# Performance work log

Measured on AMD Instinct MI355X. Metric: run time of the kernel, lower is better.

## Reference

```python
import jax, jax.numpy as jnp
import numpy as np

B, C_IN, C_OUT, H, W = 4, 128, 64, 64, 64


def setup_inputs() -> dict:
    key = jax.random.key(0)
    ks = jax.random.split(key, 10)
    s = 0.05
    return {
        "x": jax.random.normal(ks[0], (B, C_IN, H, W), dtype=jnp.float32),
        "Wf": jax.random.normal(ks[1], (C_OUT, C_IN), dtype=jnp.float32) * s,
        "bf": jax.random.normal(ks[2], (C_OUT,), dtype=jnp.float32) * s,
        "Wg": jax.random.normal(ks[3], (C_OUT, C_IN), dtype=jnp.float32) * s,
        "bg": jax.random.normal(ks[4], (C_OUT,), dtype=jnp.float32) * s,
        "Wh": jax.random.normal(ks[5], (C_OUT, C_IN), dtype=jnp.float32) * s,
        "bh": jax.random.normal(ks[6], (C_OUT,), dtype=jnp.float32) * s,
        "Wa": jax.random.normal(ks[7], (C_OUT, C_OUT), dtype=jnp.float32) * s,
        "ba": jax.random.normal(ks[8], (C_OUT,), dtype=jnp.float32) * s,
        "gamma": jnp.ones((1,), dtype=jnp.float32),
    }


def _conv1x1(W, b, xf):
    # xf: [B, Cin, N] -> [B, Cout, N]
    return jnp.einsum('oc,bcn->bon', W, xf) + b[None, :, None]


def reference(x, Wf, bf, Wg, bg, Wh, bh, Wa, ba, gamma):
    nb, nc, imgh, imgw = x.shape
    xf = x.reshape(nb, nc, imgh * imgw)            # [B, Cin, N]
    f = _conv1x1(Wf, bf, xf)                       # [B, Co, N]
    g = _conv1x1(Wg, bg, xf)
    h = _conv1x1(Wh, bh, xf)
    # s = f^T @ g : [B, N, N]
    s = jnp.einsum('bon,bom->bnm', f, g)
    beta = jax.nn.softmax(s, axis=-1)              # softmax over keys (last dim)
    # o = beta @ h^T : [B, N, Co]
    o = jnp.einsum('bnm,bom->bno', beta, h)
    o = jnp.swapaxes(o, 1, 2)                      # [B, Co, N]
    o = _conv1x1(Wa, ba, o)                        # attn_conv 1x1
    out = gamma * o.reshape(nb, -1, imgh, imgw)    # [B, Co, H, W]
    return out
```

## Files before the change

kernel.cpp:

```cpp
#include <hip/hip_runtime.h>
#include <math.h>

#define BATCH 4
#define CIN   128
#define CO    64
#define NPIX  4096
#define LOG2E 1.4426950408889634f

typedef unsigned int   uint_t;
typedef unsigned short ushort_t;
typedef __bf16 bfx8 __attribute__((ext_vector_type(8)));
typedef float  f32x4  __attribute__((ext_vector_type(4)));
typedef float  f32x16 __attribute__((ext_vector_type(16)));

#define MFMA(a,b,c)   __builtin_amdgcn_mfma_f32_16x16x32_bf16((a),(b),(c),0,0,0)
#define MFMA32(a,b,c) __builtin_amdgcn_mfma_f32_32x32x16_bf16((a),(b),(c),0,0,0)
#define BC8(x) __builtin_bit_cast(bfx8,(x))

#if __has_builtin(__builtin_amdgcn_exp2f)
#define EXP2(x) __builtin_amdgcn_exp2f(x)
#else
#define EXP2(x) exp2f(x)
#endif

static __device__ __forceinline__ ushort_t f2bf(float f) {
    uint_t u = __builtin_bit_cast(uint_t, f);
    u = (u + 0x7fffu + ((u >> 16) & 1u)) >> 16;
    return (ushort_t)u;
}
static __device__ __forceinline__ float bf2f(ushort_t h) {
    return __builtin_bit_cast(float, (uint_t)h << 16);
}
static __device__ __forceinline__ uint_t pk2(float a, float b) {
    return (uint_t)f2bf(a) | ((uint_t)f2bf(b) << 16);
}
static __device__ __forceinline__ uint_t cvtpk(float lo, float hi) {
    uint_t r;
    asm("v_cvt_pk_bf16_f32 %0, %1, %2" : "=v"(r) : "v"(lo), "v"(hi));
    return r;
}
static __device__ __forceinline__ void gload16(const void* g, void* l) {
    __builtin_amdgcn_global_load_lds(
        (const __attribute__((address_space(1))) void*)g,
        (__attribute__((address_space(3))) void*)l, 16, 0, 0);
}

__global__ __launch_bounds__(256) void wconv_kernel(
    const float* __restrict__ Wf, const float* __restrict__ Wg,
    const float* __restrict__ Wh, const float* __restrict__ Wa,
    ushort_t* __restrict__ Wb)
{
    int gid = blockIdx.x * 256 + threadIdx.x;
    for (int e = gid; e < 28672; e += 4096) {
        float v;
        if      (e < 8192)  v = Wf[e];
        else if (e < 16384) v = Wg[e - 8192];
        else if (e < 24576) v = Wh[e - 16384];
        else                v = Wa[e - 24576];
        Wb[e] = f2bf(v);
    }
}

__global__ __launch_bounds__(256) void proj_kernel(
    const float* __restrict__ x, const ushort_t* __restrict__ Wb,
    const float* __restrict__ bf_, const float* __restrict__ bg_, const float* __restrict__ bh_,
    ushort_t* __restrict__ Q, ushort_t* __restrict__ K, ushort_t* __restrict__ V)
{
    int bid = blockIdx.x, b = bid >> 6, n0 = (bid & 63) << 6, t = threadIdx.x;
    int w = t >> 6, lane = t & 63, cl = lane & 15, g = (lane >> 4) & 3;

    const float* xcol = x + (size_t)b * CIN * NPIX + n0 + (w << 4) + cl;

    uint4 aq[4];
    #pragma unroll
    for (int ks = 0; ks < 4; ++ks) {
        float v[8];
        #pragma unroll
        for (int j = 0; j < 8; ++j)
            v[j] = xcol[(size_t)((ks << 5) + (g << 3) + j) * NPIX];
        uint4 a;
        a.x = pk2(v[0], v[1]);
        a.y = pk2(v[2], v[3]);
        a.z = pk2(v[4], v[5]);
        a.w = pk2(v[6], v[7]);
        aq[ks] = a;
    }

    const float* bps[3] = {bf_, bg_, bh_};
    int nb = n0 + (w << 4);

    for (int p = 0; p < 3; ++p) {
        const ushort_t* Wp = Wb + p * 8192;
        float sc = (p == 0) ? LOG2E : 1.0f;
        f32x4 acc[4];
        #pragma unroll
        for (int ot = 0; ot < 4; ++ot) acc[ot] = (f32x4){0.f,0.f,0.f,0.f};
        #pragma unroll
        for (int ks = 0; ks < 4; ++ks) {
            #pragma unroll
            for (int ot = 0; ot < 4; ++ot) {
                uint4 bq = *(const uint4*)(Wp + (((ot << 4) + cl) << 7) + (ks << 5) + (g << 3));
                acc[ot] = MFMA(BC8(aq[ks]), BC8(bq), acc[ot]);
            }
        }
        if (p < 2) {
            ushort_t* dst = (p == 0 ? Q : K) + ((size_t)b * NPIX + nb) * CO;
            #pragma unroll
            for (int ot = 0; ot < 4; ++ot) {
                float bias = bps[p][(ot << 4) + cl];
                #pragma unroll
                for (int r = 0; r < 4; ++r)
                    dst[(size_t)((g << 2) + r) * CO + (ot << 4) + cl] = f2bf((acc[ot][r] + bias) * sc);
            }
        } else {
            #pragma unroll
            for (int ot = 0; ot < 4; ++ot) {
                float bias = bps[p][(ot << 4) + cl];
                uint2 pk;
                pk.x = pk2(acc[ot][0] + bias, acc[ot][1] + bias);
                pk.y = pk2(acc[ot][2] + bias, acc[ot][3] + bias);
                ushort_t* Vd = V + (size_t)b * CO * NPIX + (size_t)((ot << 4) + cl) * NPIX + nb + (g << 2);
                *(uint2*)Vd = pk;
            }
        }
    }
}

__global__ __launch_bounds__(1024, 4) void flash_kernel(
    const ushort_t* __restrict__ Q, const ushort_t* __restrict__ K,
    const ushort_t* __restrict__ V, const ushort_t* __restrict__ Wb,
    const float* __restrict__ ba, const float* __restrict__ gamma,
    float* __restrict__ out)
{
    extern __shared__ __align__(16) char smem[];

    int orig = blockIdx.x;
    int bid = ((orig & 7) << 5) | (orig >> 3);
    int b = bid >> 6, n0 = (bid & 63) << 6, t = threadIdx.x;
    int w = t >> 6, lane = t & 63;
    int qh = w >> 3, ks = w & 7;
    int ql = lane & 31, hi = lane >> 5;

    const ushort_t* Qb = Q + ((size_t)b * NPIX + n0) * CO;
    const ushort_t* Kb = K + (size_t)b * NPIX * CO;
    const ushort_t* Vb = V + (size_t)b * CO * NPIX;

    int q = (qh << 5) + ql;
    uint4 qf[4];
    #pragma unroll
    for (int m = 0; m < 4; ++m)
        qf[m] = *(const uint4*)(Qb + q * CO + (m << 4) + (hi << 3));

    f32x16 oac0 = (f32x16)0.f, oac1 = (f32x16)0.f;
    float mreg = -INFINITY, lreg = 0.f;

    int kl = (ql & 19) | ((ql & 4) << 1) | ((ql & 8) >> 1);
    int key = (ks << 5) + kl;
    int koff[4];
    #pragma unroll
    for (int m = 0; m < 4; ++m)
        koff[m] = (key << 7) + (((((m << 1) | hi)) ^ (key & 7)) << 4);
    int voff[2][2];
    #pragma unroll
    for (int dh = 0; dh < 2; ++dh)
        #pragma unroll
        for (int kt = 0; kt < 2; ++kt) {
            int dv = (dh << 5) + ql;
            int slot = (((ks << 2) + (kt << 1) + hi)) ^ (dv & 7);
            voff[dh][kt] = 32768 + (dv << 9) + (slot << 4);
        }

    auto STAGE = [&](char* buf, int kt) {
        #pragma unroll
        for (int i = 0; i < 2; ++i) {
            int cb = (i << 10) + (w << 6);
            int ci = cb | lane;
            int kk = ci >> 3, kc = (ci & 7) ^ (kk & 7);
            gload16(Kb + (size_t)((kt << 8) + kk) * CO + (kc << 3), buf + (cb << 4));
            int d = ci >> 5, vc = (ci & 31) ^ (d & 7);
            gload16(Vb + (size_t)d * NPIX + (kt << 8) + (vc << 3), buf + 32768 + (cb << 4));
        }
    };

    auto DOTILE = [&](char* bufc) {
        uint4 kf0 = *(const uint4*)(bufc + koff[0]);
        uint4 kf1 = *(const uint4*)(bufc + koff[1]);
        uint4 kf2 = *(const uint4*)(bufc + koff[2]);
        uint4 kf3 = *(const uint4*)(bufc + koff[3]);
        f32x16 s = (f32x16)0.f;
        __builtin_amdgcn_s_setprio(1);
        s = MFMA32(BC8(kf0), BC8(qf[0]), s);
        s = MFMA32(BC8(kf1), BC8(qf[1]), s);
        s = MFMA32(BC8(kf2), BC8(qf[2]), s);
        s = MFMA32(BC8(kf3), BC8(qf[3]), s);
        __builtin_amdgcn_s_setprio(0);

        float mx = s[0];
        #pragma unroll
        for (int p = 1; p < 16; ++p) mx = fmaxf(mx, s[p]);
        mx = fmaxf(mx, __shfl_xor(mx, 32));
        if (!__all(mx <= mreg + 11.5f)) {
            float mn = fmaxf(mreg, mx);
            float r  = EXP2(mreg - mn);
            lreg *= r;
            oac0 *= r; oac1 *= r;
            mreg = mn;
        }
        float pv[16], ls = 0.f;
        #pragma unroll
        for (int p = 0; p < 16; ++p) { pv[p] = EXP2(s[p] - mreg); ls += pv[p]; }
        ls += __shfl_xor(ls, 32);
        lreg += ls;
        uint4 pb0, pb1;
        pb0.x = cvtpk(pv[0], pv[1]);  pb0.y = cvtpk(pv[2],  pv[3]);
        pb0.z = cvtpk(pv[4], pv[5]);  pb0.w = cvtpk(pv[6],  pv[7]);
        pb1.x = cvtpk(pv[8], pv[9]);  pb1.y = cvtpk(pv[10], pv[11]);
        pb1.z = cvtpk(pv[12], pv[13]); pb1.w = cvtpk(pv[14], pv[15]);

        uint4 vf00 = *(const uint4*)(bufc + voff[0][0]);
        uint4 vf01 = *(const uint4*)(bufc + voff[0][1]);
        uint4 vf10 = *(const uint4*)(bufc + voff[1][0]);
        uint4 vf11 = *(const uint4*)(bufc + voff[1][1]);
        __builtin_amdgcn_s_setprio(1);
        oac0 = MFMA32(BC8(vf00), BC8(pb0), oac0);
        oac0 = MFMA32(BC8(vf01), BC8(pb1), oac0);
        oac1 = MFMA32(BC8(vf10), BC8(pb0), oac1);
        oac1 = MFMA32(BC8(vf11), BC8(pb1), oac1);
        __builtin_amdgcn_s_setprio(0);
    };

    STAGE(smem, 0);
    __syncthreads();
    for (int i = 0; i < 16; ++i) {
        if (i + 1 < 16) STAGE(smem + (((i + 1) & 1) << 16), i + 1);
        DOTILE(smem + ((i & 1) << 16));
        __syncthreads();
    }

    float* mlb = (float*)(smem + 131072);
    float* llb = (float*)(smem + 133120);
    if (lane < 32) {
        mlb[(w << 5) + lane] = mreg;
        llb[(w << 5) + lane] = lreg;
    }
    __syncthreads();

    float M = -INFINITY;
    float mv[8];
    #pragma unroll
    for (int i = 0; i < 8; ++i) {
        mv[i] = mlb[(((qh << 3) + i) << 5) + ql];
        M = fmaxf(M, mv[i]);
    }
    float L = 0.f;
    #pragma unroll
    for (int i = 0; i < 8; ++i)
        L += EXP2(mv[i] - M) * llb[(((qh << 3) + i) << 5) + ql];
    float fac = EXP2(mreg - M) / L;
    oac0 *= fac; oac1 *= fac;

    for (int r = 0; r < 7; ++r) {
        if (ks == r) {
            #pragma unroll
            for (int dh = 0; dh < 2; ++dh)
                #pragma unroll
                for (int j2 = 0; j2 < 4; ++j2) {
                    int slot = (((j2 << 1) + hi + (dh << 3))) ^ (q & 7);
                    int off = (q << 8) + (slot << 4);
                    f32x4 v;
                    if (dh == 0) v = (f32x4){oac0[4*j2], oac0[4*j2+1], oac0[4*j2+2], oac0[4*j2+3]};
                    else         v = (f32x4){oac1[4*j2], oac1[4*j2+1], oac1[4*j2+2], oac1[4*j2+3]};
                    if (r > 0) v += *(const f32x4*)(smem + off);
                    *(f32x4*)(smem + off) = v;
                }
        }
        __syncthreads();
    }
    ushort_t* Pb = (ushort_t*)(smem + 16384);
    if (ks == 7) {
        #pragma unroll
        for (int dh = 0; dh < 2; ++dh)
            #pragma unroll
            for (int j2 = 0; j2 < 4; ++j2) {
                int slot = (((j2 << 1) + hi + (dh << 3))) ^ (q & 7);
                int off = (q << 8) + (slot << 4);
                f32x4 v;
                if (dh == 0) v = (f32x4){oac0[4*j2], oac0[4*j2+1], oac0[4*j2+2], oac0[4*j2+3]};
                else         v = (f32x4){oac1[4*j2], oac1[4*j2+1], oac1[4*j2+2], oac1[4*j2+3]};
                v += *(const f32x4*)(smem + off);
                uint2 pk;
                pk.x = pk2(v[0], v[1]);
                pk.y = pk2(v[2], v[3]);
                *(uint2*)((char*)Pb + q * 144 + (j2 << 4) + (hi << 3) + (dh << 6)) = pk;
            }
    }
    __syncthreads();

    {
        int c = lane & 15, g = (lane >> 4) & 3;
        const ushort_t* Wab = Wb + 24576;
        float gm = gamma[0];
        int ot = w >> 2, qt3 = w & 3;
        f32x4 acc2 = (f32x4){0.f,0.f,0.f,0.f};
        #pragma unroll
        for (int k2 = 0; k2 < 2; ++k2) {
            uint4 af  = *(const uint4*)(Wab + (((ot << 4) + c) << 6) + (k2 << 5) + (g << 3));
            uint4 pfq = *(const uint4*)((char*)Pb + (((qt3 << 4) + c)) * 144 + (k2 << 6) + (g << 4));
            acc2 = MFMA(BC8(af), BC8(pfq), acc2);
        }
        float* ob = out + (size_t)b * CO * NPIX + n0;
        #pragma unroll
        for (int r = 0; r < 4; ++r) {
            int o = (ot << 4) + (g << 2) + r;
            ob[(size_t)o * NPIX + (qt3 << 4) + c] = gm * (acc2[r] + ba[o]);
        }
    }
}

extern "C" void kernel_launch(void* const* d_in, const int* in_sizes, int n_in,
                              void* d_out, int out_size, void* d_ws, size_t ws_size,
                              hipStream_t stream) {
    const float* x     = (const float*)d_in[0];
    const float* Wf    = (const float*)d_in[1];
    const float* bf_   = (const float*)d_in[2];
    const float* Wg    = (const float*)d_in[3];
    const float* bg_   = (const float*)d_in[4];
    const float* Wh    = (const float*)d_in[5];
    const float* bh_   = (const float*)d_in[6];
    const float* Wa    = (const float*)d_in[7];
    const float* ba    = (const float*)d_in[8];
    const float* gamma = (const float*)d_in[9];
    float* out = (float*)d_out;

    ushort_t* Wb = (ushort_t*)d_ws;
    const size_t matb = (size_t)BATCH * NPIX * CO;
    ushort_t* Q = (ushort_t*)((char*)d_ws + 65536);
    ushort_t* K = Q + matb;
    ushort_t* V = K + matb;

    wconv_kernel<<<16, 256, 0, stream>>>(Wf, Wg, Wh, Wa, Wb);
    proj_kernel<<<BATCH * (NPIX / 64), 256, 0, stream>>>(x, Wb, bf_, bg_, bh_, Q, K, V);
    flash_kernel<<<BATCH * (NPIX / 64), 1024, 135168, stream>>>(Q, K, V, Wb, ba, gamma, out);
}
```

Baseline: 53.55 us.

## Load K/V fragments directly from global memory instead of double-buffered LDS staging

The flash kernel no longer stages 256-key K/V tiles into double-buffered shared memory with async global-to-LDS loads and per-tile barriers. Each wave now reads its MFMA fragments for K and V straight from global memory (L2-resident), and the score registers are reused in place for the exponentials. This removes the per-iteration __syncthreads and the large dynamic LDS allocation, shrinking LDS to a small static buffer for the reduction epilogue. The cost is that both query-half waves fetch the same keys, doubling cache traffic, and there is no explicit prefetch to hide global load latency.

Measured after the change: 85.24 us. 59.2% more time.

```diff
diff --git a/kernel.cpp b/kernel.cpp
--- a/kernel.cpp
+++ b/kernel.cpp
@@ -38,11 +38,6 @@
     uint_t r;
     asm("v_cvt_pk_bf16_f32 %0, %1, %2" : "=v"(r) : "v"(lo), "v"(hi));
     return r;
-}
-static __device__ __forceinline__ void gload16(const void* g, void* l) {
-    __builtin_amdgcn_global_load_lds(
-        (const __attribute__((address_space(1))) void*)g,
-        (__attribute__((address_space(3))) void*)l, 16, 0, 0);
 }
 
 __global__ __launch_bounds__(256) void wconv_kernel(
@@ -132,7 +127,7 @@
     const float* __restrict__ ba, const float* __restrict__ gamma,
     float* __restrict__ out)
 {
-    extern __shared__ __align__(16) char smem[];
+    __shared__ __align__(16) char smem[30720];
 
     int orig = blockIdx.x;
     int bid = ((orig & 7) << 5) | (orig >> 3);
@@ -155,38 +150,21 @@
     float mreg = -INFINITY, lreg = 0.f;
 
     int kl = (ql & 19) | ((ql & 4) << 1) | ((ql & 8) >> 1);
-    int key = (ks << 5) + kl;
-    int koff[4];
-    #pragma unroll
-    for (int m = 0; m < 4; ++m)
-        koff[m] = (key << 7) + (((((m << 1) | hi)) ^ (key & 7)) << 4);
-    int voff[2][2];
-    #pragma unroll
-    for (int dh = 0; dh < 2; ++dh)
-        #pragma unroll
-        for (int kt = 0; kt < 2; ++kt) {
-            int dv = (dh << 5) + ql;
-            int slot = (((ks << 2) + (kt << 1) + hi)) ^ (dv & 7);
-            voff[dh][kt] = 32768 + (dv << 9) + (slot << 4);
-        }
-
-    auto STAGE = [&](char* buf, int kt) {
-        #pragma unroll
-        for (int i = 0; i < 2; ++i) {
-            int cb = (i << 10) + (w << 6);
-            int ci = cb | lane;
-            int kk = ci >> 3, kc = (ci & 7) ^ (kk & 7);
-            gload16(Kb + (size_t)((kt << 8) + kk) * CO + (kc << 3), buf + (cb << 4));
-            int d = ci >> 5, vc = (ci & 31) ^ (d & 7);
-            gload16(Vb + (size_t)d * NPIX + (kt << 8) + (vc << 3), buf + 32768 + (cb << 4));
-        }
-    };
-
-    auto DOTILE = [&](char* bufc) {
-        uint4 kf0 = *(const uint4*)(bufc + koff[0]);
-        uint4 kf1 = *(const uint4*)(bufc + koff[1]);
-        uint4 kf2 = *(const uint4*)(bufc + koff[2]);
-        uint4 kf3 = *(const uint4*)(bufc + koff[3]);
+    const ushort_t* Kp = Kb + (size_t)(((ks << 5) + kl) * CO) + (hi << 3);
+    const ushort_t* Vp = Vb + (size_t)ql * NPIX + (ks << 5) + (hi << 3);
+
+    for (int i = 0; i < 16; ++i) {
+        const ushort_t* Kt = Kp + (size_t)i * (256 * CO);
+        const ushort_t* Vt = Vp + (i << 8);
+        uint4 kf0 = *(const uint4*)(Kt);
+        uint4 kf1 = *(const uint4*)(Kt + 16);
+        uint4 kf2 = *(const uint4*)(Kt + 32);
+        uint4 kf3 = *(const uint4*)(Kt + 48);
+        uint4 vf00 = *(const uint4*)(Vt);
+        uint4 vf01 = *(const uint4*)(Vt + 16);
+        uint4 vf10 = *(const uint4*)(Vt + (NPIX << 5));
+        uint4 vf11 = *(const uint4*)(Vt + (NPIX << 5) + 16);
+
         f32x16 s = (f32x16)0.f;
         __builtin_amdgcn_s_setprio(1);
         s = MFMA32(BC8(kf0), BC8(qf[0]), s);
@@ -206,39 +184,27 @@
             oac0 *= r; oac1 *= r;
             mreg = mn;
         }
-        float pv[16], ls = 0.f;
-        #pragma unroll
-        for (int p = 0; p < 16; ++p) { pv[p] = EXP2(s[p] - mreg); ls += pv[p]; }
+        float ls = 0.f;
+        #pragma unroll
+        for (int p = 0; p < 16; ++p) { s[p] = EXP2(s[p] - mreg); ls += s[p]; }
         ls += __shfl_xor(ls, 32);
         lreg += ls;
         uint4 pb0, pb1;
-        pb0.x = cvtpk(pv[0], pv[1]);  pb0.y = cvtpk(pv[2],  pv[3]);
-        pb0.z = cvtpk(pv[4], pv[5]);  pb0.w = cvtpk(pv[6],  pv[7]);
-        pb1.x = cvtpk(pv[8], pv[9]);  pb1.y = cvtpk(pv[10], pv[11]);
-        pb1.z = cvtpk(pv[12], pv[13]); pb1.w = cvtpk(pv[14], pv[15]);
-
-        uint4 vf00 = *(const uint4*)(bufc + voff[0][0]);
-        uint4 vf01 = *(const uint4*)(bufc + voff[0][1]);
-        uint4 vf10 = *(const uint4*)(bufc + voff[1][0]);
-        uint4 vf11 = *(const uint4*)(bufc + voff[1][1]);
+        pb0.x = cvtpk(s[0], s[1]);   pb0.y = cvtpk(s[2],  s[3]);
+        pb0.z = cvtpk(s[4], s[5]);   pb0.w = cvtpk(s[6],  s[7]);
+        pb1.x = cvtpk(s[8], s[9]);   pb1.y = cvtpk(s[10], s[11]);
+        pb1.z = cvtpk(s[12], s[13]); pb1.w = cvtpk(s[14], s[15]);
+
         __builtin_amdgcn_s_setprio(1);
         oac0 = MFMA32(BC8(vf00), BC8(pb0), oac0);
         oac0 = MFMA32(BC8(vf01), BC8(pb1), oac0);
         oac1 = MFMA32(BC8(vf10), BC8(pb0), oac1);
         oac1 = MFMA32(BC8(vf11), BC8(pb1), oac1);
         __builtin_amdgcn_s_setprio(0);
-    };
-
-    STAGE(smem, 0);
-    __syncthreads();
-    for (int i = 0; i < 16; ++i) {
-        if (i + 1 < 16) STAGE(smem + (((i + 1) & 1) << 16), i + 1);
-        DOTILE(smem + ((i & 1) << 16));
-        __syncthreads();
-    }
-
-    float* mlb = (float*)(smem + 131072);
-    float* llb = (float*)(smem + 133120);
+    }
+
+    float* mlb = (float*)(smem + 25600);
+    float* llb = (float*)(smem + 27648);
     if (lane < 32) {
         mlb[(w << 5) + lane] = mreg;
         llb[(w << 5) + lane] = lreg;
@@ -340,5 +306,5 @@
 
     wconv_kernel<<<16, 256, 0, stream>>>(Wf, Wg, Wh, Wa, Wb);
     proj_kernel<<<BATCH * (NPIX / 64), 256, 0, stream>>>(x, Wb, bf_, bg_, bh_, Q, K, V);
-    flash_kernel<<<BATCH * (NPIX / 64), 1024, 135168, stream>>>(Q, K, V, Wb, ba, gamma, out);
-}
+    flash_kernel<<<BATCH * (NPIX / 64), 1024, 0, stream>>>(Q, K, V, Wb, ba, gamma, out);
+}
```
